# Kernel tuning notes

Hardware: AMD Instinct MI355X
Metric: run time of the kernel (lower is better)

## Reference

```python
import jax, jax.numpy as jnp
import numpy as np

B, S, E, H, V, C = 64, 512, 256, 128, 50000, 2


def setup_inputs() -> dict:
    key = jax.random.key(0)
    ks = jax.random.split(key, 12)
    sentences = jax.random.randint(ks[0], (B, S), 0, V, dtype=jnp.int32)
    # sparse binary adjacency (dependency-tree-like), float for bmm
    adj = (jax.random.uniform(ks[1], (B, S, S)) < 0.05).astype(jnp.float32)
    emb_table = jax.random.normal(ks[2], (V, E), dtype=jnp.float32) * 0.02
    W1 = jax.random.normal(ks[3], (H, E), dtype=jnp.float32) * 0.05
    b1 = jnp.zeros((H,), jnp.float32)
    W2 = jax.random.normal(ks[4], (H, H), dtype=jnp.float32) * 0.05
    b2 = jnp.zeros((H,), jnp.float32)
    W3 = jax.random.normal(ks[5], (H, H), dtype=jnp.float32) * 0.05
    b3 = jnp.zeros((H,), jnp.float32)
    Wp = jax.random.normal(ks[6], (C, H), dtype=jnp.float32) * 0.05
    bp = jnp.zeros((C,), jnp.float32)
    return {"sentences": sentences, "adj": adj, "emb_table": emb_table,
            "W1": W1, "b1": b1, "W2": W2, "b2": b2, "W3": W3, "b3": b3,
            "Wp": Wp, "bp": bp}


def reference(sentences, adj, emb_table, W1, b1, W2, b2, W3, b3, Wp, bp):
    # embedding lookup (dropout is eval-mode identity)
    h = emb_table[sentences]  # [B, S, E]
    # degree normalization term (self-loop adds +1)
    deg = jnp.sum(adj, axis=-1, keepdims=True) + 1.0  # [B, S, 1]
    for W, b in ((W1, b1), (W2, b2), (W3, b3)):
        agg = jnp.einsum('bst,btd->bsd', adj, h)  # bmm(adj, h)
        # layer(agg) + layer(h) == (agg + h) @ W^T + 2b  (shared weights)
        h = ((agg + h) @ W.T + 2.0 * b) / deg
        h = jax.nn.relu(h)
    # AdaptiveMaxPool1d(1) over sequence dim
    pooled = jnp.max(h, axis=1)  # [B, H]
    logits = pooled @ Wp.T + bp  # [B, C]
    return logits
```

## Files before the change

### kernel.cpp

```cpp
#include <hip/hip_runtime.h>

typedef unsigned short ushort_t;

#define B_ 64
#define S_ 512
#define E_ 256
#define H_ 128
#define M_ (B_ * S_)
#define CAP_ 128

__global__ void k_adjidx(const float* __restrict__ adj,
                         ushort_t* __restrict__ idxl,
                         int* __restrict__ nnz,
                         float* __restrict__ invdeg) {
    int row  = blockIdx.x * 4 + (threadIdx.x >> 6);
    int lane = threadIdx.x & 63;
    const float4* arow = (const float4*)(adj + (size_t)row * S_);
    ushort_t* dst = idxl + (size_t)row * CAP_;
    int total = 0;
    #pragma unroll
    for (int c = 0; c < 2; ++c) {
        float4 v = arow[c * 64 + lane];
        float f[4] = {v.x, v.y, v.z, v.w};
        #pragma unroll
        for (int j = 0; j < 4; ++j) {
            unsigned long long m = __ballot(f[j] != 0.0f);
            if (f[j] != 0.0f) {
                int pos = total + __popcll(m & ((1ull << lane) - 1ull));
                if (pos < CAP_) dst[pos] = (ushort_t)(c * 256 + lane * 4 + j);
            }
            total += __popcll(m);
        }
    }
    if (lane == 0) {
        nnz[row] = total < CAP_ ? total : CAP_;
        invdeg[row] = 1.0f / (float)(total + 1);
    }
}

template <int K, bool GATHER, bool POOL>
__global__ __launch_bounds__(256, 1)
void k_layer(const float* __restrict__ X, const int* __restrict__ sent,
             const float* __restrict__ emb, const float* __restrict__ W,
             const ushort_t* __restrict__ idxl, const int* __restrict__ nnz,
             const float* __restrict__ invdeg, const float* __restrict__ bias,
             float* __restrict__ out) {
    __shared__ __align__(16) float Ys[S_ * 36];
    __shared__ __align__(16) float Xs[2][8 * S_];
    __shared__ __align__(16) float Wsh[2][8 * 32];

    const int tid = threadIdx.x;
    const int bid = blockIdx.x;
    const int xcd = bid & 7, slot = bid >> 3;
    const int b = xcd + 8 * (slot >> 2);
    const int cg = slot & 3;
    const int colBase = cg * 32;
    const int rowBase = b * S_;

    const int row0 = tid >> 1;
    const int kq   = (tid & 1) * 4;
    const float* xp[4];
    #pragma unroll
    for (int q = 0; q < 4; ++q) {
        const int r = row0 + 128 * q;
        const float* src;
        if (GATHER) src = emb + (size_t)sent[rowBase + r] * K;
        else        src = X + (size_t)(rowBase + r) * K;
        xp[q] = src + kq;
    }
    const int wcol = (tid >> 1) & 31;
    const float* wp = W + (size_t)(colBase + wcol) * K + kq;

    const int rg4 = tid & ~3;
    const int c0  = (tid & 3) * 8;

    float acc[8][8] = {};
    float4 g[4];
    float4 wv = {0.f, 0.f, 0.f, 0.f};

    constexpr int NC = K / 8;

    #pragma unroll
    for (int q = 0; q < 4; ++q) g[q] = *(const float4*)(xp[q]);
    if (tid < 64) wv = *(const float4*)(wp);
    #pragma unroll
    for (int q = 0; q < 4; ++q) {
        const int pr = row0 + 128 * q;
        Xs[0][(kq + 0) * 512 + pr] = g[q].x;
        Xs[0][(kq + 1) * 512 + pr] = g[q].y;
        Xs[0][(kq + 2) * 512 + pr] = g[q].z;
        Xs[0][(kq + 3) * 512 + pr] = g[q].w;
    }
    if (tid < 64) {
        Wsh[0][(kq + 0) * 32 + wcol] = wv.x;
        Wsh[0][(kq + 1) * 32 + wcol] = wv.y;
        Wsh[0][(kq + 2) * 32 + wcol] = wv.z;
        Wsh[0][(kq + 3) * 32 + wcol] = wv.w;
    }
    __syncthreads();

    #pragma unroll 1
    for (int c = 0; c < NC; ++c) {
        const int cur = c & 1;
        if (c + 1 < NC) {
            #pragma unroll
            for (int q = 0; q < 4; ++q) g[q] = *(const float4*)(xp[q] + (c + 1) * 8);
            if (tid < 64) wv = *(const float4*)(wp + (c + 1) * 8);
        }
        #pragma unroll
        for (int k = 0; k < 8; ++k) {
            const float4 xa = *(const float4*)&Xs[cur][k * 512 + rg4];
            const float4 xb = *(const float4*)&Xs[cur][k * 512 + 256 + rg4];
            const float4 wa = *(const float4*)&Wsh[cur][k * 32 + c0];
            const float4 wb = *(const float4*)&Wsh[cur][k * 32 + c0 + 4];
            const float xv[8]  = {xa.x, xa.y, xa.z, xa.w, xb.x, xb.y, xb.z, xb.w};
            const float wv8[8] = {wa.x, wa.y, wa.z, wa.w, wb.x, wb.y, wb.z, wb.w};
            #pragma unroll
            for (int i = 0; i < 8; ++i)
                #pragma unroll
                for (int j = 0; j < 8; ++j)
                    acc[i][j] += xv[i] * wv8[j];
        }
        if (c + 1 < NC) {
            const int nb = cur ^ 1;
            #pragma unroll
            for (int q = 0; q < 4; ++q) {
                const int pr = row0 + 128 * q;
                Xs[nb][(kq + 0) * 512 + pr] = g[q].x;
                Xs[nb][(kq + 1) * 512 + pr] = g[q].y;
                Xs[nb][(kq + 2) * 512 + pr] = g[q].z;
                Xs[nb][(kq + 3) * 512 + pr] = g[q].w;
            }
            if (tid < 64) {
                Wsh[nb][(kq + 0) * 32 + wcol] = wv.x;
                Wsh[nb][(kq + 1) * 32 + wcol] = wv.y;
                Wsh[nb][(kq + 2) * 32 + wcol] = wv.z;
                Wsh[nb][(kq + 3) * 32 + wcol] = wv.w;
            }
        }
        __syncthreads();
    }

    #pragma unroll
    for (int i = 0; i < 8; ++i) {
        const int r = (i < 4) ? (rg4 + i) : (256 + rg4 + i - 4);
        *(float4*)&Ys[r * 36 + c0]     = make_float4(acc[i][0], acc[i][1], acc[i][2], acc[i][3]);
        *(float4*)&Ys[r * 36 + c0 + 4] = make_float4(acc[i][4], acc[i][5], acc[i][6], acc[i][7]);
    }
    __syncthreads();

    const int rsub = tid >> 3;
    const int cc   = tid & 7;
    const float4* Ys4 = (const float4*)Ys;
    const float4 bv = *(const float4*)(bias + colBase + cc * 4);
    float4 pmax = {0.f, 0.f, 0.f, 0.f};

    #pragma unroll 1
    for (int p = 0; p < 16; ++p) {
        const int r = p * 32 + rsub;
        const int grow = rowBase + r;
        const int n = nnz[grow];
        const ushort_t* il = idxl + (size_t)grow * CAP_;
        float4 a = Ys4[r * 9 + cc];
        float4 a2 = {0.f, 0.f, 0.f, 0.f};
        int i = 0;
        for (; i + 4 <= n; i += 4) {
            const unsigned long long pk = *(const unsigned long long*)(il + i);
            const int t0 = (int)(pk & 0xffffu);
            const int t1 = (int)((pk >> 16) & 0xffffu);
            const int t2 = (int)((pk >> 32) & 0xffffu);
            const int t3 = (int)((pk >> 48) & 0xffffu);
            const float4 v0 = Ys4[t0 * 9 + cc];
            const float4 v1 = Ys4[t1 * 9 + cc];
            const float4 v2 = Ys4[t2 * 9 + cc];
            const float4 v3 = Ys4[t3 * 9 + cc];
            a.x += v0.x + v1.x;  a.y += v0.y + v1.y;
            a.z += v0.z + v1.z;  a.w += v0.w + v1.w;
            a2.x += v2.x + v3.x; a2.y += v2.y + v3.y;
            a2.z += v2.z + v3.z; a2.w += v2.w + v3.w;
        }
        for (; i < n; ++i) {
            const int t = il[i];
            const float4 v = Ys4[t * 9 + cc];
            a.x += v.x; a.y += v.y; a.z += v.z; a.w += v.w;
        }
        a.x += a2.x; a.y += a2.y; a.z += a2.z; a.w += a2.w;
        const float inv = invdeg[grow];
        float4 o;
        o.x = fmaxf((a.x + 2.0f * bv.x) * inv, 0.0f);
        o.y = fmaxf((a.y + 2.0f * bv.y) * inv, 0.0f);
        o.z = fmaxf((a.z + 2.0f * bv.z) * inv, 0.0f);
        o.w = fmaxf((a.w + 2.0f * bv.w) * inv, 0.0f);
        if (!POOL) {
            *(float4*)(out + (size_t)grow * H_ + colBase + cc * 4) = o;
        } else {
            pmax.x = fmaxf(pmax.x, o.x); pmax.y = fmaxf(pmax.y, o.y);
            pmax.z = fmaxf(pmax.z, o.z); pmax.w = fmaxf(pmax.w, o.w);
        }
    }

    if (POOL) {
        float4* smax = (float4*)Xs;
        smax[rsub * 8 + cc] = pmax;
        __syncthreads();
        if (tid < 8) {
            float4 m = smax[tid];
            #pragma unroll 8
            for (int q = 1; q < 32; ++q) {
                const float4 v = smax[q * 8 + tid];
                m.x = fmaxf(m.x, v.x); m.y = fmaxf(m.y, v.y);
                m.z = fmaxf(m.z, v.z); m.w = fmaxf(m.w, v.w);
            }
            *(float4*)(out + (size_t)b * H_ + colBase + tid * 4) = m;
        }
    }
}

__global__ void k_final(const float* __restrict__ pooled,
                        const float* __restrict__ Wp,
                        const float* __restrict__ bp,
                        float* __restrict__ out) {
    int b = blockIdx.x, j = threadIdx.x;
    float m = pooled[(size_t)b * H_ + j];
    float t0 = m * Wp[j];
    float t1 = m * Wp[H_ + j];
    #pragma unroll
    for (int off = 32; off > 0; off >>= 1) {
        t0 += __shfl_down(t0, off);
        t1 += __shfl_down(t1, off);
    }
    __shared__ float red[2][2];
    int wave = j >> 6, lane = j & 63;
    if (lane == 0) { red[0][wave] = t0; red[1][wave] = t1; }
    __syncthreads();
    if (j == 0) out[b * 2 + 0] = red[0][0] + red[0][1] + bp[0];
    if (j == 1) out[b * 2 + 1] = red[1][0] + red[1][1] + bp[1];
}

extern "C" void kernel_launch(void* const* d_in, const int* in_sizes, int n_in,
                              void* d_out, int out_size, void* d_ws, size_t ws_size,
                              hipStream_t stream) {
    const int*   sent = (const int*)d_in[0];
    const float* adj  = (const float*)d_in[1];
    const float* emb  = (const float*)d_in[2];
    const float* W1   = (const float*)d_in[3];
    const float* b1   = (const float*)d_in[4];
    const float* W2   = (const float*)d_in[5];
    const float* b2   = (const float*)d_in[6];
    const float* W3   = (const float*)d_in[7];
    const float* b3   = (const float*)d_in[8];
    const float* Wp   = (const float*)d_in[9];
    const float* bp   = (const float*)d_in[10];
    float* out = (float*)d_out;

    char* ws = (char*)d_ws;
    float*    h1     = (float*)ws;
    float*    h2     = (float*)(ws + ((size_t)16 << 20));
    char*     base   = ws + ((size_t)32 << 20);
    float*    invdeg = (float*)base;
    int*      nnz    = (int*)(base + (size_t)M_ * 4);
    ushort_t* idxl   = (ushort_t*)(base + (size_t)M_ * 8);
    float*    pooled = (float*)(base + (size_t)M_ * 8 + (size_t)M_ * CAP_ * 2);

    k_adjidx<<<M_ / 4, 256, 0, stream>>>(adj, idxl, nnz, invdeg);

    k_layer<E_, true,  false><<<256, 256, 0, stream>>>(nullptr, sent, emb, W1, idxl, nnz, invdeg, b1, h1);
    k_layer<H_, false, false><<<256, 256, 0, stream>>>(h1, nullptr, nullptr, W2, idxl, nnz, invdeg, b2, h2);
    k_layer<H_, false, true ><<<256, 256, 0, stream>>>(h2, nullptr, nullptr, W3, idxl, nnz, invdeg, b3, pooled);

    k_final<<<B_, H_, 0, stream>>>(pooled, Wp, bp, out);
}
```

Baseline: 326.8 us.

## Double block threads to 512, halve per-thread tile, prefetch sparse indices

```diff
diff --git a/kernel.cpp b/kernel.cpp
--- a/kernel.cpp
+++ b/kernel.cpp
@@ -1,6 +1,7 @@
 #include <hip/hip_runtime.h>
 
 typedef unsigned short ushort_t;
+typedef unsigned long long ull_t;
 
 #define B_ 64
 #define S_ 512
@@ -39,7 +40,7 @@
 }
 
 template <int K, bool GATHER, bool POOL>
-__global__ __launch_bounds__(256, 1)
+__global__ __launch_bounds__(512, 2)
 void k_layer(const float* __restrict__ X, const int* __restrict__ sent,
              const float* __restrict__ emb, const float* __restrict__ W,
              const ushort_t* __restrict__ idxl, const int* __restrict__ nnz,
@@ -57,16 +58,16 @@
     const int colBase = cg * 32;
     const int rowBase = b * S_;
 
-    const int row0 = tid >> 1;
-    const int kq   = (tid & 1) * 4;
-    const float* xp[4];
-    #pragma unroll
-    for (int q = 0; q < 4; ++q) {
-        const int r = row0 + 128 * q;
-        const float* src;
-        if (GATHER) src = emb + (size_t)sent[rowBase + r] * K;
-        else        src = X + (size_t)(rowBase + r) * K;
-        xp[q] = src + kq;
+    const int r0 = tid >> 1;
+    const int kq = (tid & 1) * 4;
+    const float* xp0;
+    const float* xp1;
+    if (GATHER) {
+        xp0 = emb + (size_t)sent[rowBase + r0]       * K + kq;
+        xp1 = emb + (size_t)sent[rowBase + r0 + 256] * K + kq;
+    } else {
+        xp0 = X + (size_t)(rowBase + r0)       * K + kq;
+        xp1 = X + (size_t)(rowBase + r0 + 256) * K + kq;
     }
     const int wcol = (tid >> 1) & 31;
     const float* wp = W + (size_t)(colBase + wcol) * K + kq;
@@ -74,23 +75,23 @@
     const int rg4 = tid & ~3;
     const int c0  = (tid & 3) * 8;
 
-    float acc[8][8] = {};
-    float4 g[4];
+    float acc[4][8] = {};
+    float4 g0, g1;
     float4 wv = {0.f, 0.f, 0.f, 0.f};
 
     constexpr int NC = K / 8;
 
-    #pragma unroll
-    for (int q = 0; q < 4; ++q) g[q] = *(const float4*)(xp[q]);
-    if (tid < 64) wv = *(const float4*)(wp);
-    #pragma unroll
-    for (int q = 0; q < 4; ++q) {
-        const int pr = row0 + 128 * q;
-        Xs[0][(kq + 0) * 512 + pr] = g[q].x;
-        Xs[0][(kq + 1) * 512 + pr] = g[q].y;
-        Xs[0][(kq + 2) * 512 + pr] = g[q].z;
-        Xs[0][(kq + 3) * 512 + pr] = g[q].w;
-    }
+    g0 = *(const float4*)xp0;
+    g1 = *(const float4*)xp1;
+    if (tid < 64) wv = *(const float4*)wp;
+    Xs[0][(kq + 0) * 512 + r0] = g0.x;
+    Xs[0][(kq + 1) * 512 + r0] = g0.y;
+    Xs[0][(kq + 2) * 512 + r0] = g0.z;
+    Xs[0][(kq + 3) * 512 + r0] = g0.w;
+    Xs[0][(kq + 0) * 512 + r0 + 256] = g1.x;
+    Xs[0][(kq + 1) * 512 + r0 + 256] = g1.y;
+    Xs[0][(kq + 2) * 512 + r0 + 256] = g1.z;
+    Xs[0][(kq + 3) * 512 + r0 + 256] = g1.w;
     if (tid < 64) {
         Wsh[0][(kq + 0) * 32 + wcol] = wv.x;
         Wsh[0][(kq + 1) * 32 + wcol] = wv.y;
@@ -103,34 +104,33 @@
     for (int c = 0; c < NC; ++c) {
         const int cur = c & 1;
         if (c + 1 < NC) {
-            #pragma unroll
-            for (int q = 0; q < 4; ++q) g[q] = *(const float4*)(xp[q] + (c + 1) * 8);
+            g0 = *(const float4*)(xp0 + (c + 1) * 8);
+            g1 = *(const float4*)(xp1 + (c + 1) * 8);
             if (tid < 64) wv = *(const float4*)(wp + (c + 1) * 8);
         }
         #pragma unroll
         for (int k = 0; k < 8; ++k) {
             const float4 xa = *(const float4*)&Xs[cur][k * 512 + rg4];
-            const float4 xb = *(const float4*)&Xs[cur][k * 512 + 256 + rg4];
             const float4 wa = *(const float4*)&Wsh[cur][k * 32 + c0];
             const float4 wb = *(const float4*)&Wsh[cur][k * 32 + c0 + 4];
-            const float xv[8]  = {xa.x, xa.y, xa.z, xa.w, xb.x, xb.y, xb.z, xb.w};
+            const float xv[4]  = {xa.x, xa.y, xa.z, xa.w};
             const float wv8[8] = {wa.x, wa.y, wa.z, wa.w, wb.x, wb.y, wb.z, wb.w};
             #pragma unroll
-            for (int i = 0; i < 8; ++i)
+            for (int i = 0; i < 4; ++i)
                 #pragma unroll
                 for (int j = 0; j < 8; ++j)
                     acc[i][j] += xv[i] * wv8[j];
         }
         if (c + 1 < NC) {
             const int nb = cur ^ 1;
-            #pragma unroll
-            for (int q = 0; q < 4; ++q) {
-                const int pr = row0 + 128 * q;
-                Xs[nb][(kq + 0) * 512 + pr] = g[q].x;
-                Xs[nb][(kq + 1) * 512 + pr] = g[q].y;
-                Xs[nb][(kq + 2) * 512 + pr] = g[q].z;
-                Xs[nb][(kq + 3) * 512 + pr] = g[q].w;
-            }
+            Xs[nb][(kq + 0) * 512 + r0] = g0.x;
+            Xs[nb][(kq + 1) * 512 + r0] = g0.y;
+            Xs[nb][(kq + 2) * 512 + r0] = g0.z;
+            Xs[nb][(kq + 3) * 512 + r0] = g0.w;
+            Xs[nb][(kq + 0) * 512 + r0 + 256] = g1.x;
+            Xs[nb][(kq + 1) * 512 + r0 + 256] = g1.y;
+            Xs[nb][(kq + 2) * 512 + r0 + 256] = g1.z;
+            Xs[nb][(kq + 3) * 512 + r0 + 256] = g1.w;
             if (tid < 64) {
                 Wsh[nb][(kq + 0) * 32 + wcol] = wv.x;
                 Wsh[nb][(kq + 1) * 32 + wcol] = wv.y;
@@ -142,8 +142,8 @@
     }
 
     #pragma unroll
-    for (int i = 0; i < 8; ++i) {
-        const int r = (i < 4) ? (rg4 + i) : (256 + rg4 + i - 4);
+    for (int i = 0; i < 4; ++i) {
+        const int r = rg4 + i;
         *(float4*)&Ys[r * 36 + c0]     = make_float4(acc[i][0], acc[i][1], acc[i][2], acc[i][3]);
         *(float4*)&Ys[r * 36 + c0 + 4] = make_float4(acc[i][4], acc[i][5], acc[i][6], acc[i][7]);
     }
@@ -155,17 +155,28 @@
     const float4 bv = *(const float4*)(bias + colBase + cc * 4);
     float4 pmax = {0.f, 0.f, 0.f, 0.f};
 
+    int grow = rowBase + rsub;
+    int n_cur = nnz[grow];
+    float inv_cur = invdeg[grow];
+    const ushort_t* il = idxl + (size_t)grow * CAP_;
+    ull_t pk = *(const ull_t*)il;
+
     #pragma unroll 1
-    for (int p = 0; p < 16; ++p) {
-        const int r = p * 32 + rsub;
-        const int grow = rowBase + r;
-        const int n = nnz[grow];
-        const ushort_t* il = idxl + (size_t)grow * CAP_;
+    for (int p = 0; p < 8; ++p) {
+        const int r = p * 64 + rsub;
+        int n_nxt = 0; float inv_nxt = 0.f; ull_t pk_nxt = 0;
+        const ushort_t* il_nxt = il + 64 * CAP_;
+        if (p < 7) {
+            n_nxt = nnz[grow + 64];
+            inv_nxt = invdeg[grow + 64];
+            pk_nxt = *(const ull_t*)il_nxt;
+        }
         float4 a = Ys4[r * 9 + cc];
         float4 a2 = {0.f, 0.f, 0.f, 0.f};
+        const int n = n_cur;
         int i = 0;
         for (; i + 4 <= n; i += 4) {
-            const unsigned long long pk = *(const unsigned long long*)(il + i);
+            const ull_t pk_p = *(const ull_t*)(il + i + 4);
             const int t0 = (int)(pk & 0xffffu);
             const int t1 = (int)((pk >> 16) & 0xffffu);
             const int t2 = (int)((pk >> 32) & 0xffffu);
@@ -178,6 +189,7 @@
             a.z += v0.z + v1.z;  a.w += v0.w + v1.w;
             a2.x += v2.x + v3.x; a2.y += v2.y + v3.y;
             a2.z += v2.z + v3.z; a2.w += v2.w + v3.w;
+            pk = pk_p;
         }
         for (; i < n; ++i) {
             const int t = il[i];
@@ -185,18 +197,19 @@
             a.x += v.x; a.y += v.y; a.z += v.z; a.w += v.w;
         }
         a.x += a2.x; a.y += a2.y; a.z += a2.z; a.w += a2.w;
-        const float inv = invdeg[grow];
         float4 o;
-        o.x = fmaxf((a.x + 2.0f * bv.x) * inv, 0.0f);
-        o.y = fmaxf((a.y + 2.0f * bv.y) * inv, 0.0f);
-        o.z = fmaxf((a.z + 2.0f * bv.z) * inv, 0.0f);
-        o.w = fmaxf((a.w + 2.0f * bv.w) * inv, 0.0f);
+        o.x = fmaxf((a.x + 2.0f * bv.x) * inv_cur, 0.0f);
+        o.y = fmaxf((a.y + 2.0f * bv.y) * inv_cur, 0.0f);
+        o.z = fmaxf((a.z + 2.0f * bv.z) * inv_cur, 0.0f);
+        o.w = fmaxf((a.w + 2.0f * bv.w) * inv_cur, 0.0f);
         if (!POOL) {
-            *(float4*)(out + (size_t)grow * H_ + colBase + cc * 4) = o;
+            *(float4*)(out + (size_t)(rowBase + r) * H_ + colBase + cc * 4) = o;
         } else {
             pmax.x = fmaxf(pmax.x, o.x); pmax.y = fmaxf(pmax.y, o.y);
             pmax.z = fmaxf(pmax.z, o.z); pmax.w = fmaxf(pmax.w, o.w);
         }
+        grow += 64; il = il_nxt;
+        n_cur = n_nxt; inv_cur = inv_nxt; pk = pk_nxt;
     }
 
     if (POOL) {
@@ -206,7 +219,7 @@
         if (tid < 8) {
             float4 m = smax[tid];
             #pragma unroll 8
-            for (int q = 1; q < 32; ++q) {
+            for (int q = 1; q < 64; ++q) {
                 const float4 v = smax[q * 8 + tid];
                 m.x = fmaxf(m.x, v.x); m.y = fmaxf(m.y, v.y);
                 m.z = fmaxf(m.z, v.z); m.w = fmaxf(m.w, v.w);
@@ -264,9 +277,9 @@
 
     k_adjidx<<<M_ / 4, 256, 0, stream>>>(adj, idxl, nnz, invdeg);
 
-    k_layer<E_, true,  false><<<256, 256, 0, stream>>>(nullptr, sent, emb, W1, idxl, nnz, invdeg, b1, h1);
-    k_layer<H_, false, false><<<256, 256, 0, stream>>>(h1, nullptr, nullptr, W2, idxl, nnz, invdeg, b2, h2);
-    k_layer<H_, false, true ><<<256, 256, 0, stream>>>(h2, nullptr, nullptr, W3, idxl, nnz, invdeg, b3, pooled);
+    k_layer<E_, true,  false><<<256, 512, 0, stream>>>(nullptr, sent, emb, W1, idxl, nnz, invdeg, b1, h1);
+    k_layer<H_, false, false><<<256, 512, 0, stream>>>(h1, nullptr, nullptr, W2, idxl, nnz, invdeg, b2, h2);
+    k_layer<H_, false, true ><<<256, 512, 0, stream>>>(h2, nullptr, nullptr, W3, idxl, nnz, invdeg, b3, pooled);
 
     k_final<<<B_, H_, 0, stream>>>(pooled, Wp, bp, out);
 }
```

New measurement: 279.9 us. -14.4%, faster.

## Split layer kernel into 16-column tiles with 512 threads and more blocks

Applied to the files above, without the earlier changes.

```diff
diff --git a/kernel.cpp b/kernel.cpp
--- a/kernel.cpp
+++ b/kernel.cpp
@@ -1,6 +1,7 @@
 #include <hip/hip_runtime.h>
 
 typedef unsigned short ushort_t;
+typedef unsigned long long ull_t;
 
 #define B_ 64
 #define S_ 512
@@ -39,63 +40,56 @@
 }
 
 template <int K, bool GATHER, bool POOL>
-__global__ __launch_bounds__(256, 1)
+__global__ __launch_bounds__(512, 4)
 void k_layer(const float* __restrict__ X, const int* __restrict__ sent,
              const float* __restrict__ emb, const float* __restrict__ W,
              const ushort_t* __restrict__ idxl, const int* __restrict__ nnz,
              const float* __restrict__ invdeg, const float* __restrict__ bias,
              float* __restrict__ out) {
-    __shared__ __align__(16) float Ys[S_ * 36];
+    __shared__ __align__(16) float Ys[S_ * 20];
     __shared__ __align__(16) float Xs[2][8 * S_];
-    __shared__ __align__(16) float Wsh[2][8 * 32];
+    __shared__ __align__(16) float Wsh[2][8 * 16];
 
     const int tid = threadIdx.x;
     const int bid = blockIdx.x;
-    const int xcd = bid & 7, slot = bid >> 3;
-    const int b = xcd + 8 * (slot >> 2);
-    const int cg = slot & 3;
-    const int colBase = cg * 32;
+    const int b  = (bid & 7) + 8 * (bid >> 6);
+    const int cg = (bid >> 3) & 7;
+    const int colBase = cg * 16;
     const int rowBase = b * S_;
 
-    const int row0 = tid >> 1;
-    const int kq   = (tid & 1) * 4;
-    const float* xp[4];
-    #pragma unroll
-    for (int q = 0; q < 4; ++q) {
-        const int r = row0 + 128 * q;
-        const float* src;
-        if (GATHER) src = emb + (size_t)sent[rowBase + r] * K;
-        else        src = X + (size_t)(rowBase + r) * K;
-        xp[q] = src + kq;
-    }
-    const int wcol = (tid >> 1) & 31;
-    const float* wp = W + (size_t)(colBase + wcol) * K + kq;
+    const float* xp;
+    if (GATHER) xp = emb + (size_t)sent[rowBase + tid] * K;
+    else        xp = X + (size_t)(rowBase + tid) * K;
+
+    const int wcol = tid & 15;
+    const int kq4  = (tid >> 4) * 4;
+    const float* wp = W + (size_t)(colBase + wcol) * K + kq4;
 
     const int rg4 = tid & ~3;
-    const int c0  = (tid & 3) * 8;
-
-    float acc[8][8] = {};
-    float4 g[4];
+    const int c0  = (tid & 3) * 4;
+
+    float acc[4][4] = {};
+    float4 g0, g1;
     float4 wv = {0.f, 0.f, 0.f, 0.f};
 
     constexpr int NC = K / 8;
 
-    #pragma unroll
-    for (int q = 0; q < 4; ++q) g[q] = *(const float4*)(xp[q]);
-    if (tid < 64) wv = *(const float4*)(wp);
-    #pragma unroll
-    for (int q = 0; q < 4; ++q) {
-        const int pr = row0 + 128 * q;
-        Xs[0][(kq + 0) * 512 + pr] = g[q].x;
-        Xs[0][(kq + 1) * 512 + pr] = g[q].y;
-        Xs[0][(kq + 2) * 512 + pr] = g[q].z;
-        Xs[0][(kq + 3) * 512 + pr] = g[q].w;
-    }
-    if (tid < 64) {
-        Wsh[0][(kq + 0) * 32 + wcol] = wv.x;
-        Wsh[0][(kq + 1) * 32 + wcol] = wv.y;
-        Wsh[0][(kq + 2) * 32 + wcol] = wv.z;
-        Wsh[0][(kq + 3) * 32 + wcol] = wv.w;
+    g0 = *(const float4*)(xp);
+    g1 = *(const float4*)(xp + 4);
+    if (tid < 32) wv = *(const float4*)(wp);
+    Xs[0][0 * 512 + tid] = g0.x;
+    Xs[0][1 * 512 + tid] = g0.y;
+    Xs[0][2 * 512 + tid] = g0.z;
+    Xs[0][3 * 512 + tid] = g0.w;
+    Xs[0][4 * 512 + tid] = g1.x;
+    Xs[0][5 * 512 + tid] = g1.y;
+    Xs[0][6 * 512 + tid] = g1.z;
+    Xs[0][7 * 512 + tid] = g1.w;
+    if (tid < 32) {
+        Wsh[0][(kq4 + 0) * 16 + wcol] = wv.x;
+        Wsh[0][(kq4 + 1) * 16 + wcol] = wv.y;
+        Wsh[0][(kq4 + 2) * 16 + wcol] = wv.z;
+        Wsh[0][(kq4 + 3) * 16 + wcol] = wv.w;
     }
     __syncthreads();
 
@@ -103,89 +97,114 @@
     for (int c = 0; c < NC; ++c) {
         const int cur = c & 1;
         if (c + 1 < NC) {
-            #pragma unroll
-            for (int q = 0; q < 4; ++q) g[q] = *(const float4*)(xp[q] + (c + 1) * 8);
-            if (tid < 64) wv = *(const float4*)(wp + (c + 1) * 8);
+            g0 = *(const float4*)(xp + (c + 1) * 8);
+            g1 = *(const float4*)(xp + (c + 1) * 8 + 4);
+            if (tid < 32) wv = *(const float4*)(wp + (c + 1) * 8);
         }
         #pragma unroll
         for (int k = 0; k < 8; ++k) {
             const float4 xa = *(const float4*)&Xs[cur][k * 512 + rg4];
-            const float4 xb = *(const float4*)&Xs[cur][k * 512 + 256 + rg4];
-            const float4 wa = *(const float4*)&Wsh[cur][k * 32 + c0];
-            const float4 wb = *(const float4*)&Wsh[cur][k * 32 + c0 + 4];
-            const float xv[8]  = {xa.x, xa.y, xa.z, xa.w, xb.x, xb.y, xb.z, xb.w};
-            const float wv8[8] = {wa.x, wa.y, wa.z, wa.w, wb.x, wb.y, wb.z, wb.w};
+            const float4 wa = *(const float4*)&Wsh[cur][k * 16 + c0];
+            const float xv[4] = {xa.x, xa.y, xa.z, xa.w};
+            const float wf[4] = {wa.x, wa.y, wa.z, wa.w};
             #pragma unroll
-            for (int i = 0; i < 8; ++i)
+            for (int i = 0; i < 4; ++i)
                 #pragma unroll
-                for (int j = 0; j < 8; ++j)
-                    acc[i][j] += xv[i] * wv8[j];
+                for (int j = 0; j < 4; ++j)
+                    acc[i][j] += xv[i] * wf[j];
         }
         if (c + 1 < NC) {
             const int nb = cur ^ 1;
-            #pragma unroll
-            for (int q = 0; q < 4; ++q) {
-                const int pr = row0 + 128 * q;
-                Xs[nb][(kq + 0) * 512 + pr] = g[q].x;
-                Xs[nb][(kq + 1) * 512 + pr] = g[q].y;
-                Xs[nb][(kq + 2) * 512 + pr] = g[q].z;
-                Xs[nb][(kq + 3) * 512 + pr] = g[q].w;
+            Xs[nb][0 * 512 + tid] = g0.x;
+            Xs[nb][1 * 512 + tid] = g0.y;
+            Xs[nb][2 * 512 + tid] = g0.z;
+            Xs[nb][3 * 512 + tid] = g0.w;
+            Xs[nb][4 * 512 + tid] = g1.x;
+            Xs[nb][5 * 512 + tid] = g1.y;
+            Xs[nb][6 * 512 + tid] = g1.z;
+            Xs[nb][7 * 512 + tid] = g1.w;
+            if (tid < 32) {
+                Wsh[nb][(kq4 + 0) * 16 + wcol] = wv.x;
+                Wsh[nb][(kq4 + 1) * 16 + wcol] = wv.y;
+                Wsh[nb][(kq4 + 2) * 16 + wcol] = wv.z;
+                Wsh[nb][(kq4 + 3) * 16 + wcol] = wv.w;
             }
-            if (tid < 64) {
-                Wsh[nb][(kq + 0) * 32 + wcol] = wv.x;
-                Wsh[nb][(kq + 1) * 32 + wcol] = wv.y;
-                Wsh[nb][(kq + 2) * 32 + wcol] = wv.z;
-                Wsh[nb][(kq + 3) * 32 + wcol] = wv.w;
-            }
         }
         __syncthreads();
     }
 
     #pragma unroll
-    for (int i = 0; i < 8; ++i) {
-        const int r = (i < 4) ? (rg4 + i) : (256 + rg4 + i - 4);
-        *(float4*)&Ys[r * 36 + c0]     = make_float4(acc[i][0], acc[i][1], acc[i][2], acc[i][3]);
-        *(float4*)&Ys[r * 36 + c0 + 4] = make_float4(acc[i][4], acc[i][5], acc[i][6], acc[i][7]);
-    }
+    for (int i = 0; i < 4; ++i)
+        *(float4*)&Ys[(rg4 + i) * 20 + c0] =
+            make_float4(acc[i][0], acc[i][1], acc[i][2], acc[i][3]);
     __syncthreads();
 
-    const int rsub = tid >> 3;
-    const int cc   = tid & 7;
+    const int rsub = tid >> 2;
+    const int cc   = tid & 3;
     const float4* Ys4 = (const float4*)Ys;
     const float4 bv = *(const float4*)(bias + colBase + cc * 4);
     float4 pmax = {0.f, 0.f, 0.f, 0.f};
 
     #pragma unroll 1
-    for (int p = 0; p < 16; ++p) {
-        const int r = p * 32 + rsub;
+    for (int p = 0; p < 4; ++p) {
+        const int r = p * 128 + rsub;
         const int grow = rowBase + r;
         const int n = nnz[grow];
+        const float inv = invdeg[grow];
         const ushort_t* il = idxl + (size_t)grow * CAP_;
-        float4 a = Ys4[r * 9 + cc];
+        float4 a = Ys4[r * 5 + cc];
         float4 a2 = {0.f, 0.f, 0.f, 0.f};
         int i = 0;
-        for (; i + 4 <= n; i += 4) {
-            const unsigned long long pk = *(const unsigned long long*)(il + i);
-            const int t0 = (int)(pk & 0xffffu);
-            const int t1 = (int)((pk >> 16) & 0xffffu);
-            const int t2 = (int)((pk >> 32) & 0xffffu);
-            const int t3 = (int)((pk >> 48) & 0xffffu);
-            const float4 v0 = Ys4[t0 * 9 + cc];
-            const float4 v1 = Ys4[t1 * 9 + cc];
-            const float4 v2 = Ys4[t2 * 9 + cc];
-            const float4 v3 = Ys4[t3 * 9 + cc];
+        #pragma unroll 1
+        for (; i + 8 <= n; i += 8) {
+            const ull_t pka = *(const ull_t*)(il + i);
+            const ull_t pkb = *(const ull_t*)(il + i + 4);
+            const int t0 = (int)(pka & 0xffffu);
+            const int t1 = (int)((pka >> 16) & 0xffffu);
+            const int t2 = (int)((pka >> 32) & 0xffffu);
+            const int t3 = (int)(pka >> 48);
+            const int t4 = (int)(pkb & 0xffffu);
+            const int t5 = (int)((pkb >> 16) & 0xffffu);
+            const int t6 = (int)((pkb >> 32) & 0xffffu);
+            const int t7 = (int)(pkb >> 48);
+            const float4 v0 = Ys4[t0 * 5 + cc];
+            const float4 v1 = Ys4[t1 * 5 + cc];
+            const float4 v2 = Ys4[t2 * 5 + cc];
+            const float4 v3 = Ys4[t3 * 5 + cc];
+            const float4 v4 = Ys4[t4 * 5 + cc];
+            const float4 v5 = Ys4[t5 * 5 + cc];
+            const float4 v6 = Ys4[t6 * 5 + cc];
+            const float4 v7 = Ys4[t7 * 5 + cc];
             a.x += v0.x + v1.x;  a.y += v0.y + v1.y;
             a.z += v0.z + v1.z;  a.w += v0.w + v1.w;
             a2.x += v2.x + v3.x; a2.y += v2.y + v3.y;
             a2.z += v2.z + v3.z; a2.w += v2.w + v3.w;
+            a.x += v4.x + v5.x;  a.y += v4.y + v5.y;
+            a.z += v4.z + v5.z;  a.w += v4.w + v5.w;
+            a2.x += v6.x + v7.x; a2.y += v6.y + v7.y;
+            a2.z += v6.z + v7.z; a2.w += v6.w + v7.w;
+        }
+        for (; i + 4 <= n; i += 4) {
+            const ull_t pka = *(const ull_t*)(il + i);
+            const int t0 = (int)(pka & 0xffffu);
+            const int t1 = (int)((pka >> 16) & 0xffffu);
+            const int t2 = (int)((pka >> 32) & 0xffffu);
+            const int t3 = (int)(pka >> 48);
+            const float4 v0 = Ys4[t0 * 5 + cc];
+            const float4 v1 = Ys4[t1 * 5 + cc];
+            const float4 v2 = Ys4[t2 * 5 + cc];
+            const float4 v3 = Ys4[t3 * 5 + cc];
+            a.x += v0.x + v1.x;  a.y += v0.y + v1.y;
+            a.z += v0.z + v1.z;  a.w += v0.w + v1.w;
+            a2.x += v2.x + v3.x; a2.y += v2.y + v3.y;
+            a2.z += v2.z + v3.z; a2.w += v2.w + v3.w;
         }
         for (; i < n; ++i) {
             const int t = il[i];
-            const float4 v = Ys4[t * 9 + cc];
+            const float4 v = Ys4[t * 5 + cc];
             a.x += v.x; a.y += v.y; a.z += v.z; a.w += v.w;
         }
         a.x += a2.x; a.y += a2.y; a.z += a2.z; a.w += a2.w;
-        const float inv = invdeg[grow];
         float4 o;
         o.x = fmaxf((a.x + 2.0f * bv.x) * inv, 0.0f);
         o.y = fmaxf((a.y + 2.0f * bv.y) * inv, 0.0f);
@@ -201,13 +220,25 @@
 
     if (POOL) {
         float4* smax = (float4*)Xs;
-        smax[rsub * 8 + cc] = pmax;
+        smax[tid] = pmax;
         __syncthreads();
-        if (tid < 8) {
-            float4 m = smax[tid];
-            #pragma unroll 8
-            for (int q = 1; q < 32; ++q) {
-                const float4 v = smax[q * 8 + tid];
+        if (tid < 64) {
+            const int gg = tid >> 2, c2 = tid & 3;
+            float4 m = smax[gg * 4 + c2];
+            #pragma unroll
+            for (int j = 1; j < 8; ++j) {
+                const float4 v = smax[(gg + 16 * j) * 4 + c2];
+                m.x = fmaxf(m.x, v.x); m.y = fmaxf(m.y, v.y);
+                m.z = fmaxf(m.z, v.z); m.w = fmaxf(m.w, v.w);
+            }
+            smax[512 + gg * 4 + c2] = m;
+        }
+        __syncthreads();
+        if (tid < 4) {
+            float4 m = smax[512 + tid];
+            #pragma unroll
+            for (int g = 1; g < 16; ++g) {
+                const float4 v = smax[512 + g * 4 + tid];
                 m.x = fmaxf(m.x, v.x); m.y = fmaxf(m.y, v.y);
                 m.z = fmaxf(m.z, v.z); m.w = fmaxf(m.w, v.w);
             }
@@ -264,9 +295,9 @@
 
     k_adjidx<<<M_ / 4, 256, 0, stream>>>(adj, idxl, nnz, invdeg);
 
-    k_layer<E_, true,  false><<<256, 256, 0, stream>>>(nullptr, sent, emb, W1, idxl, nnz, invdeg, b1, h1);
-    k_layer<H_, false, false><<<256, 256, 0, stream>>>(h1, nullptr, nullptr, W2, idxl, nnz, invdeg, b2, h2);
-    k_layer<H_, false, true ><<<256, 256, 0, stream>>>(h2, nullptr, nullptr, W3, idxl, nnz, invdeg, b3, pooled);
+    k_layer<E_, true,  false><<<512, 512, 0, stream>>>(nullptr, sent, emb, W1, idxl, nnz, invdeg, b1, h1);
+    k_layer<H_, false, false><<<512, 512, 0, stream>>>(h1, nullptr, nullptr, W2, idxl, nnz, invdeg, b2, h2);
+    k_layer<H_, false, true ><<<512, 512, 0, stream>>>(h2, nullptr, nullptr, W3, idxl, nnz, invdeg, b3, pooled);
 
     k_final<<<B_, H_, 0, stream>>>(pooled, Wp, bp, out);
 }
```

Measured after the change: 279.1 us. 14.6% less time.
